# Optimization experiments

Measured on AMD Instinct MI355X. Metric: run time of the kernel, lower is better.

## Reference

```python
import jax, jax.numpy as jnp
import numpy as np

NUM_NODES = 20000
EMB_DIM = 128
HIDDEN = 64
NUM_RELS = 8
NUM_CLASSES = 16
HEADS = 3
NUM_EDGES = 640000
NEG_SLOPE = 0.2


def setup_inputs() -> dict:
    key = jax.random.key(0)
    ks = jax.random.split(key, 12)
    edge_index = jax.random.randint(ks[0], (2, NUM_EDGES), 0, NUM_NODES, dtype=jnp.int32)
    edge_type = jax.random.randint(ks[1], (NUM_EDGES,), 0, NUM_RELS, dtype=jnp.int32)
    s1 = 1.0 / np.sqrt(EMB_DIM)
    s2 = 1.0 / np.sqrt(HIDDEN)
    return {
        "emb": jax.random.normal(ks[2], (NUM_NODES, EMB_DIM), jnp.float32),
        "w1": jax.random.normal(ks[3], (NUM_RELS, EMB_DIM, HEADS * HIDDEN), jnp.float32) * s1,
        "q1": jax.random.normal(ks[4], (HEADS * HIDDEN, HEADS), jnp.float32) * s2,
        "k1": jax.random.normal(ks[5], (HEADS * HIDDEN, HEADS), jnp.float32) * s2,
        "b1": jnp.zeros((HIDDEN,), jnp.float32),
        "w2": jax.random.normal(ks[6], (NUM_RELS, HIDDEN, HEADS * NUM_CLASSES), jnp.float32) * s2,
        "q2": jax.random.normal(ks[7], (HEADS * NUM_CLASSES, HEADS), jnp.float32) * 0.1,
        "k2": jax.random.normal(ks[8], (HEADS * NUM_CLASSES, HEADS), jnp.float32) * 0.1,
        "b2": jnp.zeros((NUM_CLASSES,), jnp.float32),
        "edge_index": edge_index,
        "edge_type": edge_type,
    }


def _rgat_conv(x, w, q, k, b, src, dst, edge_type, heads, out_ch):
    # Per-relation node transform [R, N, heads*out]; equivalent to x_e @ w[edge_type[e]]
    n = x.shape[0]
    xr = jnp.einsum('nd,rdo->rno', x, w)
    out_i = xr[edge_type, dst]  # [E, heads*out] (destination, x_i)
    out_j = xr[edge_type, src]  # [E, heads*out] (source, x_j)
    # additive self-attention with dim=1: alpha [E, heads]
    alpha = jax.nn.leaky_relu(out_i @ q + out_j @ k, negative_slope=NEG_SLOPE)
    # across-relation segment softmax over destination index (PyG utils.softmax)
    amax = jax.ops.segment_max(alpha, dst, num_segments=n)
    amax = jnp.where(jnp.isneginf(amax), 0.0, amax)
    ex = jnp.exp(alpha - amax[dst])
    denom = jax.ops.segment_sum(ex, dst, num_segments=n)
    alpha = ex / (denom[dst] + 1e-16)
    # weighted messages, scatter-add aggregation
    msg = alpha[:, :, None] * out_j.reshape(-1, heads, out_ch)  # [E, heads, out]
    aggr = jax.ops.segment_sum(msg, dst, num_segments=n)  # [N, heads, out]
    # concat=False -> mean over heads, then bias [out]
    return aggr.mean(axis=1) + b


def reference(emb, w1, q1, k1, b1, w2, q2, k2, b2, edge_index, edge_type):
    src, dst = edge_index[0], edge_index[1]
    x1 = _rgat_conv(emb, w1, q1, k1, b1, src, dst, edge_type, HEADS, HIDDEN)
    x2 = jax.nn.relu(x1)
    x3 = _rgat_conv(x2, w2, q2, k2, b2, src, dst, edge_type, HEADS, NUM_CLASSES)
    return jax.nn.sigmoid(x3)
```

## Files before the change

kernel.cpp:

```cpp
#include <hip/hip_runtime.h>
#include <hip/hip_bf16.h>
#include <math.h>

#define N_NODES 20000
#define EMB 128
#define HID 64
#define RELS 8
#define CLS 16
#define N_EDGES 640000
#define NEG 0.2f
#define NKEYS (N_NODES * RELS)
#define SCAN_CHUNK 1024
#define SCAN_NBLK ((NKEYS + SCAN_CHUNK - 1) / SCAN_CHUNK)

typedef unsigned short ushort_t;
typedef __attribute__((ext_vector_type(8))) short bf16x8;
typedef __attribute__((ext_vector_type(8))) unsigned short ushort8_t;
typedef __attribute__((ext_vector_type(4))) unsigned short ushort4_t;
typedef __attribute__((ext_vector_type(4))) float f32x4;

__device__ __forceinline__ float b2f(ushort_t u) {
    return __uint_as_float(((unsigned int)u) << 16);
}
__device__ __forceinline__ ushort_t f2b(float f) {
    __hip_bfloat16 h = __float2bfloat16(f);
    return *reinterpret_cast<ushort_t*>(&h);
}

__device__ __forceinline__ void prep_cvt(int i, const float* __restrict__ in, ushort_t* __restrict__ outp) {
    float4 v = *(const float4*)&in[(size_t)i * 4];
    ushort4 o;
    o.x = f2b(v.x); o.y = f2b(v.y); o.z = f2b(v.z); o.w = f2b(v.w);
    *(ushort4*)&outp[(size_t)i * 4] = o;
}

template <int D, int OUT>
__device__ __forceinline__ void prep_wqk(int tid, const float* __restrict__ w, const float* __restrict__ q,
                                         const float* __restrict__ k, ushort_t* __restrict__ wqkt) {
    int c = tid / D, i = tid % D;
    int r = c / 6, j = c % 6;
    const float* qk = (j < 3) ? q : k;
    int jj = (j < 3) ? j : j - 3;
    const float* wrow = w + ((size_t)r * D + i) * OUT;
    float s = 0.f;
    for (int o = 0; o < OUT; o++) s += wrow[o] * qk[o * 3 + jj];
    wqkt[(size_t)c * D + i] = f2b(s);
}

template <int D, int OC>
__device__ __forceinline__ void prep_wagg(int tid, const float* __restrict__ w, ushort_t* __restrict__ outp) {
    const int KT = RELS * 3 * D;
    int kidx = tid % KT;
    int o = tid / KT;
    int r = kidx / (3 * D), h = (kidx / D) % 3, i = kidx % D;
    outp[tid] = f2b(w[((size_t)r * D + i) * (3 * OC) + h * OC + o]);
}

#define PREP_N0 (N_NODES * EMB / 4)
#define PREP_N1 (48 * 128)
#define PREP_N2 (48 * 64)
#define PREP_N3 (64 * 3072)
#define PREP_N4 (16 * 1536)
#define PREP_TOT (PREP_N0 + PREP_N1 + PREP_N2 + PREP_N3 + PREP_N4)

__global__ __launch_bounds__(256) void k_prep(const float* __restrict__ emb, ushort_t* __restrict__ emb_b,
                                              const float* __restrict__ w1, const float* __restrict__ q1,
                                              const float* __restrict__ k1, ushort_t* __restrict__ wqkt1,
                                              const float* __restrict__ w2, const float* __restrict__ q2,
                                              const float* __restrict__ k2, ushort_t* __restrict__ wqkt2,
                                              ushort_t* __restrict__ wagg1, ushort_t* __restrict__ wagg2) {
    int tid = blockIdx.x * 256 + threadIdx.x;
    if (tid < PREP_N0) { prep_cvt(tid, emb, emb_b); return; }
    tid -= PREP_N0;
    if (tid < PREP_N1) { prep_wqk<128, 192>(tid, w1, q1, k1, wqkt1); return; }
    tid -= PREP_N1;
    if (tid < PREP_N2) { prep_wqk<64, 48>(tid, w2, q2, k2, wqkt2); return; }
    tid -= PREP_N2;
    if (tid < PREP_N3) { prep_wagg<128, 64>(tid, w1, wagg1); return; }
    tid -= PREP_N3;
    if (tid < PREP_N4) { prep_wagg<64, 16>(tid, w2, wagg2); return; }
}

__global__ __launch_bounds__(256) void k_count(const int* __restrict__ dst, const int* __restrict__ et,
                                               int* __restrict__ counts) {
    int e = blockIdx.x * blockDim.x + threadIdx.x;
    if (e < N_EDGES) atomicAdd(&counts[dst[e] * 8 + et[e]], 1);
}

__global__ __launch_bounds__(256) void k_scanA(const int* __restrict__ counts, int* __restrict__ keyoff,
                                               int* __restrict__ blocksum) {
    __shared__ int part[256];
    int b = blockIdx.x, tid = threadIdx.x;
    int base = b * SCAN_CHUNK + tid * 4;
    int4 c = make_int4(0, 0, 0, 0);
    if (base + 3 < NKEYS) c = *(const int4*)&counts[base];
    else {
        if (base + 0 < NKEYS) c.x = counts[base + 0];
        if (base + 1 < NKEYS) c.y = counts[base + 1];
        if (base + 2 < NKEYS) c.z = counts[base + 2];
        if (base + 3 < NKEYS) c.w = counts[base + 3];
    }
    int s = c.x + c.y + c.z + c.w;
    part[tid] = s;
    __syncthreads();
    for (int off = 1; off < 256; off <<= 1) {
        int v = (tid >= off) ? part[tid - off] : 0;
        __syncthreads();
        part[tid] += v;
        __syncthreads();
    }
    int excl = part[tid] - s;
    int4 o;
    o.x = excl;
    o.y = excl + c.x;
    o.z = excl + c.x + c.y;
    o.w = excl + c.x + c.y + c.z;
    if (base + 3 < NKEYS) *(int4*)&keyoff[base] = o;
    else {
        if (base + 0 < NKEYS) keyoff[base + 0] = o.x;
        if (base + 1 < NKEYS) keyoff[base + 1] = o.y;
        if (base + 2 < NKEYS) keyoff[base + 2] = o.z;
        if (base + 3 < NKEYS) keyoff[base + 3] = o.w;
    }
    if (tid == 255) blocksum[b] = part[255];
}

__global__ __launch_bounds__(256) void k_scanB(int* __restrict__ blocksum, int* __restrict__ blockbase,
                                               int* __restrict__ keyoff) {
    __shared__ int part[256];
    int tid = threadIdx.x;
    int v0 = (tid < SCAN_NBLK) ? blocksum[tid] : 0;
    part[tid] = v0;
    __syncthreads();
    for (int off = 1; off < 256; off <<= 1) {
        int v = (tid >= off) ? part[tid - off] : 0;
        __syncthreads();
        part[tid] += v;
        __syncthreads();
    }
    if (tid < SCAN_NBLK) blockbase[tid] = part[tid] - v0;
    if (tid == 255) keyoff[NKEYS] = part[255];
}

__global__ __launch_bounds__(256) void k_scanC(const int* __restrict__ blockbase, int* __restrict__ keyoff,
                                               int* __restrict__ cursor) {
    int b = blockIdx.x, tid = threadIdx.x;
    int base = b * SCAN_CHUNK + tid * 4;
    int add = blockbase[b];
    if (base + 3 < NKEYS) {
        int4 v = *(const int4*)&keyoff[base];
        v.x += add; v.y += add; v.z += add; v.w += add;
        *(int4*)&keyoff[base] = v;
        *(int4*)&cursor[base] = v;
    } else {
        for (int j = 0; j < 4; j++) {
            if (base + j < NKEYS) {
                int v = keyoff[base + j] + add;
                keyoff[base + j] = v;
                cursor[base + j] = v;
            }
        }
    }
}

__global__ __launch_bounds__(256) void k_scatter(const int* __restrict__ src, const int* __restrict__ dst,
                                                 const int* __restrict__ et, int* __restrict__ cursor,
                                                 int* __restrict__ srcs) {
    int e = blockIdx.x * blockDim.x + threadIdx.x;
    if (e < N_EDGES) {
        int p = atomicAdd(&cursor[dst[e] * 8 + et[e]], 1);
        srcs[p] = src[e];
    }
}

template <int K, int KCH, int N, int MREP, int NREP>
__global__ __launch_bounds__(256) void k_mfma_gemm(const ushort_t* __restrict__ A, const ushort_t* __restrict__ Bt,
                                                   float* __restrict__ outp, int M) {
    const int wid = threadIdx.x >> 6;
    const int lane = threadIdx.x & 63;
    const int m0 = blockIdx.x * (4 * MREP * 16) + wid * (MREP * 16);
    const int kbase = blockIdx.y * KCH;
    const int l15 = lane & 15;
    const int kq = (lane >> 4) * 8;

    f32x4 acc[MREP][NREP] = {};
    for (int kk = kbase; kk < kbase + KCH; kk += 32) {
        bf16x8 a[MREP], b[NREP];
#pragma unroll
        for (int i = 0; i < MREP; i++) {
            int row = m0 + i * 16 + l15;
            row = row < M ? row : M - 1;
            a[i] = *(const bf16x8*)&A[(size_t)row * K + kk + kq];
        }
#pragma unroll
        for (int j = 0; j < NREP; j++) b[j] = *(const bf16x8*)&Bt[(size_t)(j * 16 + l15) * K + kk + kq];
#pragma unroll
        for (int i = 0; i < MREP; i++)
#pragma unroll
            for (int j = 0; j < NREP; j++)
                acc[i][j] = __builtin_amdgcn_mfma_f32_16x16x32_bf16(a[i], b[j], acc[i][j], 0, 0, 0);
    }
    float* op = outp + (size_t)blockIdx.y * M * N;
    const int r4 = (lane >> 4) * 4;
#pragma unroll
    for (int i = 0; i < MREP; i++) {
#pragma unroll
        for (int j = 0; j < NREP; j++) {
#pragma unroll
            for (int g = 0; g < 4; g++) {
                int row = m0 + i * 16 + r4 + g;
                if (row < M) op[(size_t)row * N + j * 16 + l15] = acc[i][j][g];
            }
        }
    }
}

__device__ __forceinline__ void edge_alpha(int s_idx, const int (&ko)[9], const int* __restrict__ srcs,
                                           const float* __restrict__ qkd, const float* __restrict__ qbase,
                                           float& a0, float& a1, float& a2, int& sv) {
    int r = 0;
#pragma unroll
    for (int j = 1; j < 8; j++) r += (s_idx >= ko[j]) ? 1 : 0;
    sv = srcs[s_idx];
    const float* kd = qkd + (size_t)sv * 48 + r * 6 + 3;
    const float* qd = qbase + r * 6;
    float t0 = qd[0] + kd[0], t1 = qd[1] + kd[1], t2 = qd[2] + kd[2];
    a0 = t0 > 0.f ? t0 : NEG * t0;
    a1 = t1 > 0.f ? t1 : NEG * t1;
    a2 = t2 > 0.f ? t2 : NEG * t2;
}

__global__ __launch_bounds__(256) void k_stats(const int* __restrict__ keyoff, const int* __restrict__ srcs,
                                               const float* __restrict__ qkd, float4* __restrict__ svw) {
    int node = blockIdx.x * 4 + (threadIdx.x >> 6);
    int lane = threadIdx.x & 63;
    int ko[9];
#pragma unroll
    for (int j = 0; j < 9; j++) ko[j] = keyoff[node * 8 + j];
    int beg = ko[0], end = ko[8], deg = end - beg;
    if (deg == 0) return;
    const float* qbase = qkd + (size_t)node * 48;

    if (deg <= 64) {
        float a0 = -INFINITY, a1 = -INFINITY, a2 = -INFINITY;
        int sv = 0;
        if (lane < deg) edge_alpha(beg + lane, ko, srcs, qkd, qbase, a0, a1, a2, sv);
        float m0 = a0, m1 = a1, m2 = a2;
#pragma unroll
        for (int off = 32; off >= 1; off >>= 1) {
            m0 = fmaxf(m0, __shfl_xor(m0, off));
            m1 = fmaxf(m1, __shfl_xor(m1, off));
            m2 = fmaxf(m2, __shfl_xor(m2, off));
        }
        float e0 = 0.f, e1 = 0.f, e2 = 0.f;
        if (lane < deg) {
            e0 = expf(a0 - m0);
            e1 = expf(a1 - m1);
            e2 = expf(a2 - m2);
        }
        float s0 = e0, s1 = e1, s2 = e2;
#pragma unroll
        for (int off = 32; off >= 1; off >>= 1) {
            s0 += __shfl_xor(s0, off);
            s1 += __shfl_xor(s1, off);
            s2 += __shfl_xor(s2, off);
        }
        float i0 = 1.f / (3.f * (s0 + 1e-16f));
        float i1 = 1.f / (3.f * (s1 + 1e-16f));
        float i2 = 1.f / (3.f * (s2 + 1e-16f));
        if (lane < deg)
            svw[beg + lane] = make_float4(__int_as_float(sv), e0 * i0, e1 * i1, e2 * i2);
    } else {
        float m0 = -INFINITY, m1 = -INFINITY, m2 = -INFINITY;
        for (int i = beg + lane; i < end; i += 64) {
            float a0, a1, a2; int sv;
            edge_alpha(i, ko, srcs, qkd, qbase, a0, a1, a2, sv);
            m0 = fmaxf(m0, a0); m1 = fmaxf(m1, a1); m2 = fmaxf(m2, a2);
        }
#pragma unroll
        for (int off = 32; off >= 1; off >>= 1) {
            m0 = fmaxf(m0, __shfl_xor(m0, off));
            m1 = fmaxf(m1, __shfl_xor(m1, off));
            m2 = fmaxf(m2, __shfl_xor(m2, off));
        }
        float s0 = 0.f, s1 = 0.f, s2 = 0.f;
        for (int i = beg + lane; i < end; i += 64) {
            float a0, a1, a2; int sv;
            edge_alpha(i, ko, srcs, qkd, qbase, a0, a1, a2, sv);
            s0 += expf(a0 - m0); s1 += expf(a1 - m1); s2 += expf(a2 - m2);
        }
#pragma unroll
        for (int off = 32; off >= 1; off >>= 1) {
            s0 += __shfl_xor(s0, off);
            s1 += __shfl_xor(s1, off);
            s2 += __shfl_xor(s2, off);
        }
        float i0 = 1.f / (3.f * (s0 + 1e-16f));
        float i1 = 1.f / (3.f * (s1 + 1e-16f));
        float i2 = 1.f / (3.f * (s2 + 1e-16f));
        for (int i = beg + lane; i < end; i += 64) {
            float a0, a1, a2; int sv;
            edge_alpha(i, ko, srcs, qkd, qbase, a0, a1, a2, sv);
            svw[i] = make_float4(__int_as_float(sv), expf(a0 - m0) * i0, expf(a1 - m1) * i1, expf(a2 - m2) * i2);
        }
    }
}

#define PADK1 408
__global__ __launch_bounds__(256) void k_fused1(const int* __restrict__ keyoff, const float4* __restrict__ svw,
                                                const ushort_t* __restrict__ x, const ushort_t* __restrict__ wagg,
                                                float* __restrict__ part) {
    __shared__ ushort_t lt[16][PADK1];
    const int tid = threadIdx.x;
    const int w = tid >> 6, lane = tid & 63;
    const int q15 = lane & 15, kq = (lane >> 4) * 8;
    const int l15 = lane & 15;
    const int nbase = blockIdx.x * 16;
    const int r = blockIdx.y;
    const int mynode = w * 4 + (lane >> 4);
    const int key = (nbase + mynode) * 8 + r;

    const int beg = keyoff[key], end = keyoff[key + 1];
    const int deg = end - beg;
    float a0[8] = {}, a1[8] = {}, a2[8] = {};
    if (deg > 0) {
        float4 sw0 = svw[beg];
        float4 sw1;
        {
            int s = beg + 1;
            sw1 = svw[s < end ? s : beg];
            if (1 >= deg) { sw1.y = 0.f; sw1.z = 0.f; sw1.w = 0.f; }
        }
        ushort8_t xv0 = *(const ushort8_t*)&x[(size_t)__float_as_int(sw0.x) * 128 + q15 * 8];
        for (int i = 0; i < deg; i++) {
            float4 sw2;
            {
                int s = beg + i + 2;
                sw2 = svw[s < end ? s : beg];
                if (i + 2 >= deg) { sw2.y = 0.f; sw2.z = 0.f; sw2.w = 0.f; }
            }
            ushort8_t xv1 = *(const ushort8_t*)&x[(size_t)__float_as_int(sw1.x) * 128 + q15 * 8];
#pragma unroll
            for (int c = 0; c < 8; c++) {
                float f = b2f(xv0[c]);
                a0[c] += sw0.y * f;
                a1[c] += sw0.z * f;
                a2[c] += sw0.w * f;
            }
            sw0 = sw1;
            sw1 = sw2;
            xv0 = xv1;
        }
    }
    ushort8_t o0, o1, o2;
#pragma unroll
    for (int c = 0; c < 8; c++) {
        o0[c] = f2b(a0[c]);
        o1[c] = f2b(a1[c]);
        o2[c] = f2b(a2[c]);
    }
    *(ushort8_t*)&lt[mynode][0 * 128 + q15 * 8] = o0;
    *(ushort8_t*)&lt[mynode][1 * 128 + q15 * 8] = o1;
    *(ushort8_t*)&lt[mynode][2 * 128 + q15 * 8] = o2;
    __syncthreads();

    f32x4 acc = {};
#pragma unroll
    for (int ks = 0; ks < 12; ks++) {
        bf16x8 av = *(const bf16x8*)&lt[l15][ks * 32 + kq];
        bf16x8 bv = *(const bf16x8*)&wagg[(size_t)(w * 16 + l15) * 3072 + r * 384 + ks * 32 + kq];
        acc = __builtin_amdgcn_mfma_f32_16x16x32_bf16(av, bv, acc, 0, 0, 0);
    }
    float* op = part + (size_t)r * N_NODES * 64;
    const int r4 = (lane >> 4) * 4;
#pragma unroll
    for (int g = 0; g < 4; g++) {
        int row = nbase + r4 + g;
        op[(size_t)row * 64 + w * 16 + l15] = acc[g];
    }
}

#define PADK2 208
__global__ __launch_bounds__(256) void k_fused2(const int* __restrict__ keyoff, const float4* __restrict__ svw,
                                                const ushort_t* __restrict__ x2in, const ushort_t* __restrict__ wagg,
                                                float* __restrict__ part) {
    __shared__ ushort_t lt[16][PADK2];
    const int tid = threadIdx.x;
    const int w = tid >> 6, lane = tid & 63;
    const int q15 = lane & 15, kq = (lane >> 4) * 8;
    const int l15 = lane & 15;
    const int nbase = blockIdx.x * 16;
    const int r = blockIdx.y;
    const int mynode = w * 4 + (lane >> 4);
    const int key = (nbase + mynode) * 8 + r;

    const int beg = keyoff[key], end = keyoff[key + 1];
    const int deg = end - beg;
    float a0[4] = {}, a1[4] = {}, a2[4] = {};
    if (deg > 0) {
        float4 sw0 = svw[beg];
        float4 sw1;
        {
            int s = beg + 1;
            sw1 = svw[s < end ? s : beg];
            if (1 >= deg) { sw1.y = 0.f; sw1.z = 0.f; sw1.w = 0.f; }
        }
        ushort4_t xv0 = *(const ushort4_t*)&x2in[(size_t)__float_as_int(sw0.x) * 64 + q15 * 4];
        for (int i = 0; i < deg; i++) {
            float4 sw2;
            {
                int s = beg + i + 2;
                sw2 = svw[s < end ? s : beg];
                if (i + 2 >= deg) { sw2.y = 0.f; sw2.z = 0.f; sw2.w = 0.f; }
            }
            ushort4_t xv1 = *(const ushort4_t*)&x2in[(size_t)__float_as_int(sw1.x) * 64 + q15 * 4];
#pragma unroll
            for (int c = 0; c < 4; c++) {
                float f = b2f(xv0[c]);
                a0[c] += sw0.y * f;
                a1[c] += sw0.z * f;
                a2[c] += sw0.w * f;
            }
            sw0 = sw1;
            sw1 = sw2;
            xv0 = xv1;
        }
    }
    ushort4_t o0, o1, o2;
#pragma unroll
    for (int c = 0; c < 4; c++) {
        o0[c] = f2b(a0[c]);
        o1[c] = f2b(a1[c]);
        o2[c] = f2b(a2[c]);
    }
    *(ushort4_t*)&lt[mynode][0 * 64 + q15 * 4] = o0;
    *(ushort4_t*)&lt[mynode][1 * 64 + q15 * 4] = o1;
    *(ushort4_t*)&lt[mynode][2 * 64 + q15 * 4] = o2;
    __syncthreads();

    if (w == 0) {
        f32x4 acc = {};
#pragma unroll
        for (int ks = 0; ks < 6; ks++) {
            bf16x8 av = *(const bf16x8*)&lt[l15][ks * 32 + kq];
            bf16x8 bv = *(const bf16x8*)&wagg[(size_t)l15 * 1536 + r * 192 + ks * 32 + kq];
            acc = __builtin_amdgcn_mfma_f32_16x16x32_bf16(av, bv, acc, 0, 0, 0);
        }
        const int r4 = (lane >> 4) * 4;
#pragma unroll
        for (int g = 0; g < 4; g++)
            part[(size_t)r * N_NODES * 16 + (size_t)(nbase + r4 + g) * 16 + l15] = acc[g];
    }
}

__global__ __launch_bounds__(256) void k_reduce1(const float* __restrict__ part, const float* __restrict__ bias,
                                                 ushort_t* __restrict__ x2) {
    int idx = blockIdx.x * blockDim.x + threadIdx.x;
    const int MN = N_NODES * 64;
    if (idx >= MN) return;
    float s = bias[idx & 63];
#pragma unroll
    for (int r = 0; r < 8; r++) s += part[idx + (size_t)r * MN];
    x2[idx] = f2b(s > 0.f ? s : 0.f);
}

__global__ __launch_bounds__(256) void k_reduce2(const float* __restrict__ part, const float* __restrict__ bias,
                                                 float* __restrict__ outp) {
    int idx = blockIdx.x * blockDim.x + threadIdx.x;
    const int MN = N_NODES * 16;
    if (idx >= MN) return;
    float s = bias[idx & 15];
#pragma unroll
    for (int r = 0; r < 8; r++) s += part[idx + (size_t)r * MN];
    outp[idx] = 1.f / (1.f + expf(-s));
}

extern "C" void kernel_launch(void* const* d_in, const int* in_sizes, int n_in, void* d_out, int out_size,
                              void* d_ws, size_t ws_size, hipStream_t stream) {
    const float* emb = (const float*)d_in[0];
    const float* w1 = (const float*)d_in[1];
    const float* q1 = (const float*)d_in[2];
    const float* k1 = (const float*)d_in[3];
    const float* b1 = (const float*)d_in[4];
    const float* w2 = (const float*)d_in[5];
    const float* q2 = (const float*)d_in[6];
    const float* k2 = (const float*)d_in[7];
    const float* b2 = (const float*)d_in[8];
    const int* eidx = (const int*)d_in[9];
    const int* etype = (const int*)d_in[10];
    const int* srcv = eidx;
    const int* dstv = eidx + N_EDGES;
    float* out = (float*)d_out;

    char* p = (char*)d_ws;
    auto alloc = [&](size_t bytes) -> void* {
        void* q = p;
        p += (bytes + 255) & ~(size_t)255;
        return q;
    };
    int* counts = (int*)alloc((size_t)NKEYS * 4);
    int* keyoff = (int*)alloc((size_t)(NKEYS + 1) * 4);
    int* cursor = (int*)alloc((size_t)NKEYS * 4);
    int* blocksum = (int*)alloc((size_t)SCAN_NBLK * 4);
    int* blockbase = (int*)alloc((size_t)SCAN_NBLK * 4);
    int* srcs = (int*)alloc((size_t)N_EDGES * 4);
    float4* svw = (float4*)alloc((size_t)N_EDGES * 16);
    ushort_t* emb_b = (ushort_t*)alloc((size_t)N_NODES * EMB * 2);
    ushort_t* wqkt1 = (ushort_t*)alloc((size_t)48 * 128 * 2);
    ushort_t* wagg1 = (ushort_t*)alloc((size_t)64 * 3072 * 2);
    ushort_t* wqkt2 = (ushort_t*)alloc((size_t)48 * 64 * 2);
    ushort_t* wagg2 = (ushort_t*)alloc((size_t)16 * 1536 * 2);
    float* qkd = (float*)alloc((size_t)N_NODES * 48 * 4);
    ushort_t* x2 = (ushort_t*)alloc((size_t)N_NODES * 64 * 2);
    float* partials = (float*)alloc((size_t)8 * N_NODES * 64 * 4);

    k_prep<<<(PREP_TOT + 255) / 256, 256, 0, stream>>>(emb, emb_b, w1, q1, k1, wqkt1, w2, q2, k2, wqkt2, wagg1,
                                                       wagg2);

    hipMemsetAsync(counts, 0, (size_t)NKEYS * 4, stream);
    k_count<<<(N_EDGES + 255) / 256, 256, 0, stream>>>(dstv, etype, counts);
    k_scanA<<<SCAN_NBLK, 256, 0, stream>>>(counts, keyoff, blocksum);
    k_scanB<<<1, 256, 0, stream>>>(blocksum, blockbase, keyoff);
    k_scanC<<<SCAN_NBLK, 256, 0, stream>>>(blockbase, keyoff, cursor);
    k_scatter<<<(N_EDGES + 255) / 256, 256, 0, stream>>>(srcv, dstv, etype, cursor, srcs);

    k_mfma_gemm<128, 128, 48, 1, 3><<<dim3(313, 1), 256, 0, stream>>>(emb_b, wqkt1, qkd, N_NODES);
    k_stats<<<N_NODES / 4, 256, 0, stream>>>(keyoff, srcs, qkd, svw);
    k_fused1<<<dim3(N_NODES / 16, 8), 256, 0, stream>>>(keyoff, svw, emb_b, wagg1, partials);
    k_reduce1<<<(N_NODES * 64 + 255) / 256, 256, 0, stream>>>(partials, b1, x2);

    k_mfma_gemm<64, 64, 48, 1, 3><<<dim3(313, 1), 256, 0, stream>>>(x2, wqkt2, qkd, N_NODES);
    k_stats<<<N_NODES / 4, 256, 0, stream>>>(keyoff, srcs, qkd, svw);
    k_fused2<<<dim3(N_NODES / 16, 8), 256, 0, stream>>>(keyoff, svw, x2, wagg2, partials);
    k_reduce2<<<(N_NODES * 16 + 255) / 256, 256, 0, stream>>>(partials, b2, out);
}
```

Before: 243.8 us.

## Stage first gathered neighbor rows into LDS via global_load_lds before aggregation

In both fused aggregation kernels, each wave issues asynchronous global-to-LDS loads for up to 8 source rows per (node, relation) key up front, then waits once and accumulates from LDS. Edges beyond 8 fall back to direct global loads without the previous software prefetch pipeline. This aims to expose more memory-level parallelism for the irregular gather instead of a serial dependent-load chain. It adds LDS usage (which may lower occupancy) and a full vmcnt wait before any compute.

```diff
diff --git a/kernel.cpp b/kernel.cpp
--- a/kernel.cpp
+++ b/kernel.cpp
@@ -12,6 +12,7 @@
 #define NKEYS (N_NODES * RELS)
 #define SCAN_CHUNK 1024
 #define SCAN_NBLK ((NKEYS + SCAN_CHUNK - 1) / SCAN_CHUNK)
+#define S1ROWS 8
 
 typedef unsigned short ushort_t;
 typedef __attribute__((ext_vector_type(8))) short bf16x8;
@@ -25,6 +26,11 @@
 __device__ __forceinline__ ushort_t f2b(float f) {
     __hip_bfloat16 h = __float2bfloat16(f);
     return *reinterpret_cast<ushort_t*>(&h);
+}
+
+__device__ __forceinline__ void gload_lds16(const ushort_t* g, ushort_t* l) {
+    __builtin_amdgcn_global_load_lds((const __attribute__((address_space(1))) void*)g,
+                                     (__attribute__((address_space(3))) void*)l, 16, 0, 0);
 }
 
 __device__ __forceinline__ void prep_cvt(int i, const float* __restrict__ in, ushort_t* __restrict__ outp) {
@@ -307,9 +313,10 @@
 }
 
 #define PADK1 408
-__global__ __launch_bounds__(256) void k_fused1(const int* __restrict__ keyoff, const float4* __restrict__ svw,
-                                                const ushort_t* __restrict__ x, const ushort_t* __restrict__ wagg,
-                                                float* __restrict__ part) {
+__global__ __launch_bounds__(256) void k_fused1(const int* __restrict__ keyoff, const int* __restrict__ srcs,
+                                                const float4* __restrict__ svw, const ushort_t* __restrict__ x,
+                                                const ushort_t* __restrict__ wagg, float* __restrict__ part) {
+    __shared__ ushort_t stage[4][32][128];
     __shared__ ushort_t lt[16][PADK1];
     const int tid = threadIdx.x;
     const int w = tid >> 6, lane = tid & 63;
@@ -317,39 +324,54 @@
     const int l15 = lane & 15;
     const int nbase = blockIdx.x * 16;
     const int r = blockIdx.y;
-    const int mynode = w * 4 + (lane >> 4);
+    const int ln16 = lane >> 4;
+    const int mynode = w * 4 + ln16;
     const int key = (nbase + mynode) * 8 + r;
-
     const int beg = keyoff[key], end = keyoff[key + 1];
     const int deg = end - beg;
+
+#pragma unroll
+    for (int qq = 0; qq < 4; qq++) {
+        int kqk = (nbase + w * 4 + qq) * 8 + r;
+        int b = keyoff[kqk];
+        int en = keyoff[kqk + 1];
+        int nst = en - b;
+        nst = nst < S1ROWS ? nst : S1ROWS;
+#pragma unroll
+        for (int ii = 0; ii < 2; ii++) {
+            if (ii * 4 < nst) {
+                int jloc = ii * 4 + ln16;
+                int j = b + (jloc < nst ? jloc : 0);
+                int sj = srcs[j];
+                gload_lds16(&x[(size_t)sj * 128 + q15 * 8], &stage[w][qq * 8 + ii * 4][0]);
+            }
+        }
+    }
+    asm volatile("s_waitcnt vmcnt(0)" ::: "memory");
+    __builtin_amdgcn_sched_barrier(0);
+
     float a0[8] = {}, a1[8] = {}, a2[8] = {};
-    if (deg > 0) {
-        float4 sw0 = svw[beg];
-        float4 sw1;
-        {
-            int s = beg + 1;
-            sw1 = svw[s < end ? s : beg];
-            if (1 >= deg) { sw1.y = 0.f; sw1.z = 0.f; sw1.w = 0.f; }
-        }
-        ushort8_t xv0 = *(const ushort8_t*)&x[(size_t)__float_as_int(sw0.x) * 128 + q15 * 8];
-        for (int i = 0; i < deg; i++) {
-            float4 sw2;
-            {
-                int s = beg + i + 2;
-                sw2 = svw[s < end ? s : beg];
-                if (i + 2 >= deg) { sw2.y = 0.f; sw2.z = 0.f; sw2.w = 0.f; }
-            }
-            ushort8_t xv1 = *(const ushort8_t*)&x[(size_t)__float_as_int(sw1.x) * 128 + q15 * 8];
-#pragma unroll
-            for (int c = 0; c < 8; c++) {
-                float f = b2f(xv0[c]);
-                a0[c] += sw0.y * f;
-                a1[c] += sw0.z * f;
-                a2[c] += sw0.w * f;
-            }
-            sw0 = sw1;
-            sw1 = sw2;
-            xv0 = xv1;
+    const int nst = deg < S1ROWS ? deg : S1ROWS;
+    for (int j = 0; j < nst; j++) {
+        float4 sw = svw[beg + j];
+        ushort8_t xv = *(const ushort8_t*)&stage[w][ln16 * 8 + j][q15 * 8];
+#pragma unroll
+        for (int c = 0; c < 8; c++) {
+            float f = b2f(xv[c]);
+            a0[c] += sw.y * f;
+            a1[c] += sw.z * f;
+            a2[c] += sw.w * f;
+        }
+    }
+    for (int s = beg + S1ROWS; s < end; s++) {
+        float4 sw = svw[s];
+        ushort8_t xv = *(const ushort8_t*)&x[(size_t)__float_as_int(sw.x) * 128 + q15 * 8];
+#pragma unroll
+        for (int c = 0; c < 8; c++) {
+            float f = b2f(xv[c]);
+            a0[c] += sw.y * f;
+            a1[c] += sw.z * f;
+            a2[c] += sw.w * f;
         }
     }
     ushort8_t o0, o1, o2;
@@ -381,9 +403,10 @@
 }
 
 #define PADK2 208
-__global__ __launch_bounds__(256) void k_fused2(const int* __restrict__ keyoff, const float4* __restrict__ svw,
-                                                const ushort_t* __restrict__ x2in, const ushort_t* __restrict__ wagg,
-                                                float* __restrict__ part) {
+__global__ __launch_bounds__(256) void k_fused2(const int* __restrict__ keyoff, const int* __restrict__ srcs,
+                                                const float4* __restrict__ svw, const ushort_t* __restrict__ x2in,
+                                                const ushort_t* __restrict__ wagg, float* __restrict__ part) {
+    __shared__ ushort_t stage[4][32][64];
     __shared__ ushort_t lt[16][PADK2];
     const int tid = threadIdx.x;
     const int w = tid >> 6, lane = tid & 63;
@@ -391,39 +414,52 @@
     const int l15 = lane & 15;
     const int nbase = blockIdx.x * 16;
     const int r = blockIdx.y;
-    const int mynode = w * 4 + (lane >> 4);
+    const int ln16 = lane >> 4;
+    const int mynode = w * 4 + ln16;
     const int key = (nbase + mynode) * 8 + r;
-
     const int beg = keyoff[key], end = keyoff[key + 1];
     const int deg = end - beg;
+
+    const int e8 = lane >> 3;
+    const int c8 = lane & 7;
+#pragma unroll
+    for (int qq = 0; qq < 4; qq++) {
+        int kqk = (nbase + w * 4 + qq) * 8 + r;
+        int b = keyoff[kqk];
+        int en = keyoff[kqk + 1];
+        int nst = en - b;
+        nst = nst < S1ROWS ? nst : S1ROWS;
+        if (nst > 0) {
+            int j = b + (e8 < nst ? e8 : 0);
+            int sj = srcs[j];
+            gload_lds16(&x2in[(size_t)sj * 64 + c8 * 8], &stage[w][qq * 8][0]);
+        }
+    }
+    asm volatile("s_waitcnt vmcnt(0)" ::: "memory");
+    __builtin_amdgcn_sched_barrier(0);
+
     float a0[4] = {}, a1[4] = {}, a2[4] = {};
-    if (deg > 0) {
-        float4 sw0 = svw[beg];
-        float4 sw1;
-        {
-            int s = beg + 1;
-            sw1 = svw[s < end ? s : beg];
-            if (1 >= deg) { sw1.y = 0.f; sw1.z = 0.f; sw1.w = 0.f; }
-        }
-        ushort4_t xv0 = *(const ushort4_t*)&x2in[(size_t)__float_as_int(sw0.x) * 64 + q15 * 4];
-        for (int i = 0; i < deg; i++) {
-            float4 sw2;
-            {
-                int s = beg + i + 2;
-                sw2 = svw[s < end ? s : beg];
-                if (i + 2 >= deg) { sw2.y = 0.f; sw2.z = 0.f; sw2.w = 0.f; }
-            }
-            ushort4_t xv1 = *(const ushort4_t*)&x2in[(size_t)__float_as_int(sw1.x) * 64 + q15 * 4];
-#pragma unroll
-            for (int c = 0; c < 4; c++) {
-                float f = b2f(xv0[c]);
-                a0[c] += sw0.y * f;
-                a1[c] += sw0.z * f;
-                a2[c] += sw0.w * f;
-            }
-            sw0 = sw1;
-            sw1 = sw2;
-            xv0 = xv1;
+    const int nst = deg < S1ROWS ? deg : S1ROWS;
+    for (int j = 0; j < nst; j++) {
+        float4 sw = svw[beg + j];
+        ushort4_t xv = *(const ushort4_t*)&stage[w][ln16 * 8 + j][q15 * 4];
+#pragma unroll
+        for (int c = 0; c < 4; c++) {
+            float f = b2f(xv[c]);
+            a0[c] += sw.y * f;
+            a1[c] += sw.z * f;
+            a2[c] += sw.w * f;
+        }
+    }
+    for (int s = beg + S1ROWS; s < end; s++) {
+        float4 sw = svw[s];
+        ushort4_t xv = *(const ushort4_t*)&x2in[(size_t)__float_as_int(sw.x) * 64 + q15 * 4];
+#pragma unroll
+        for (int c = 0; c < 4; c++) {
+            float f = b2f(xv[c]);
+            a0[c] += sw.y * f;
+            a1[c] += sw.z * f;
+            a2[c] += sw.w * f;
         }
     }
     ushort4_t o0, o1, o2;
@@ -526,11 +562,11 @@
 
     k_mfma_gemm<128, 128, 48, 1, 3><<<dim3(313, 1), 256, 0, stream>>>(emb_b, wqkt1, qkd, N_NODES);
     k_stats<<<N_NODES / 4, 256, 0, stream>>>(keyoff, srcs, qkd, svw);
-    k_fused1<<<dim3(N_NODES / 16, 8), 256, 0, stream>>>(keyoff, svw, emb_b, wagg1, partials);
+    k_fused1<<<dim3(N_NODES / 16, 8), 256, 0, stream>>>(keyoff, srcs, svw, emb_b, wagg1, partials);
     k_reduce1<<<(N_NODES * 64 + 255) / 256, 256, 0, stream>>>(partials, b1, x2);
 
     k_mfma_gemm<64, 64, 48, 1, 3><<<dim3(313, 1), 256, 0, stream>>>(x2, wqkt2, qkd, N_NODES);
     k_stats<<<N_NODES / 4, 256, 0, stream>>>(keyoff, srcs, qkd, svw);
-    k_fused2<<<dim3(N_NODES / 16, 8), 256, 0, stream>>>(keyoff, svw, x2, wagg2, partials);
+    k_fused2<<<dim3(N_NODES / 16, 8), 256, 0, stream>>>(keyoff, srcs, svw, x2, wagg2, partials);
     k_reduce2<<<(N_NODES * 16 + 255) / 256, 256, 0, stream>>>(partials, b2, out);
 }
```

Result: slower. 299.7 us (+22.9%).

## Split layer-1 edge gather across two wave groups per node-relation key

Applied to the files above, without the earlier changes.

k_fused1 now launches 512 threads, and two groups of four waves each process alternate edges (even/odd) of every (node, relation) segment into separate LDS tiles. The MFMA stage then sums both partial tiles by issuing two MFMAs per k-step in the first four waves. The goal is to halve the serial gather chain per thread and expose more memory-level parallelism on the long dependent load loop. In exchange, half the waves sit idle during the MFMA phase, LDS use doubles, and the two partial sums are each rounded to bf16 before the GEMM.

```diff
diff --git a/kernel.cpp b/kernel.cpp
--- a/kernel.cpp
+++ b/kernel.cpp
@@ -307,49 +307,46 @@
 }
 
 #define PADK1 408
-__global__ __launch_bounds__(256) void k_fused1(const int* __restrict__ keyoff, const float4* __restrict__ svw,
+__global__ __launch_bounds__(512) void k_fused1(const int* __restrict__ keyoff, const float4* __restrict__ svw,
                                                 const ushort_t* __restrict__ x, const ushort_t* __restrict__ wagg,
                                                 float* __restrict__ part) {
-    __shared__ ushort_t lt[16][PADK1];
+    __shared__ ushort_t lt[2][16][PADK1];
     const int tid = threadIdx.x;
     const int w = tid >> 6, lane = tid & 63;
     const int q15 = lane & 15, kq = (lane >> 4) * 8;
     const int l15 = lane & 15;
     const int nbase = blockIdx.x * 16;
     const int r = blockIdx.y;
-    const int mynode = w * 4 + (lane >> 4);
+    const int mynode = (w & 3) * 4 + (lane >> 4);
+    const int p = w >> 2;
     const int key = (nbase + mynode) * 8 + r;
 
     const int beg = keyoff[key], end = keyoff[key + 1];
-    const int deg = end - beg;
     float a0[8] = {}, a1[8] = {}, a2[8] = {};
-    if (deg > 0) {
-        float4 sw0 = svw[beg];
-        float4 sw1;
-        {
-            int s = beg + 1;
-            sw1 = svw[s < end ? s : beg];
-            if (1 >= deg) { sw1.y = 0.f; sw1.z = 0.f; sw1.w = 0.f; }
-        }
-        ushort8_t xv0 = *(const ushort8_t*)&x[(size_t)__float_as_int(sw0.x) * 128 + q15 * 8];
-        for (int i = 0; i < deg; i++) {
-            float4 sw2;
-            {
-                int s = beg + i + 2;
-                sw2 = svw[s < end ? s : beg];
-                if (i + 2 >= deg) { sw2.y = 0.f; sw2.z = 0.f; sw2.w = 0.f; }
+    {
+        int sA = beg + p;
+        if (sA < end) {
+            float4 sw0 = svw[sA];
+            int sB = sA + 2;
+            float4 sw1 = svw[sB < end ? sB : beg];
+            if (sB >= end) { sw1.y = 0.f; sw1.z = 0.f; sw1.w = 0.f; }
+            ushort8_t xv0 = *(const ushort8_t*)&x[(size_t)__float_as_int(sw0.x) * 128 + q15 * 8];
+            for (int s = sA; s < end; s += 2) {
+                int sC = s + 4;
+                float4 sw2 = svw[sC < end ? sC : beg];
+                if (sC >= end) { sw2.y = 0.f; sw2.z = 0.f; sw2.w = 0.f; }
+                ushort8_t xv1 = *(const ushort8_t*)&x[(size_t)__float_as_int(sw1.x) * 128 + q15 * 8];
+#pragma unroll
+                for (int c = 0; c < 8; c++) {
+                    float f = b2f(xv0[c]);
+                    a0[c] += sw0.y * f;
+                    a1[c] += sw0.z * f;
+                    a2[c] += sw0.w * f;
+                }
+                sw0 = sw1;
+                sw1 = sw2;
+                xv0 = xv1;
             }
-            ushort8_t xv1 = *(const ushort8_t*)&x[(size_t)__float_as_int(sw1.x) * 128 + q15 * 8];
-#pragma unroll
-            for (int c = 0; c < 8; c++) {
-                float f = b2f(xv0[c]);
-                a0[c] += sw0.y * f;
-                a1[c] += sw0.z * f;
-                a2[c] += sw0.w * f;
-            }
-            sw0 = sw1;
-            sw1 = sw2;
-            xv0 = xv1;
         }
     }
     ushort8_t o0, o1, o2;
@@ -359,24 +356,28 @@
         o1[c] = f2b(a1[c]);
         o2[c] = f2b(a2[c]);
     }
-    *(ushort8_t*)&lt[mynode][0 * 128 + q15 * 8] = o0;
-    *(ushort8_t*)&lt[mynode][1 * 128 + q15 * 8] = o1;
-    *(ushort8_t*)&lt[mynode][2 * 128 + q15 * 8] = o2;
+    *(ushort8_t*)&lt[p][mynode][0 * 128 + q15 * 8] = o0;
+    *(ushort8_t*)&lt[p][mynode][1 * 128 + q15 * 8] = o1;
+    *(ushort8_t*)&lt[p][mynode][2 * 128 + q15 * 8] = o2;
     __syncthreads();
 
-    f32x4 acc = {};
-#pragma unroll
-    for (int ks = 0; ks < 12; ks++) {
-        bf16x8 av = *(const bf16x8*)&lt[l15][ks * 32 + kq];
-        bf16x8 bv = *(const bf16x8*)&wagg[(size_t)(w * 16 + l15) * 3072 + r * 384 + ks * 32 + kq];
-        acc = __builtin_amdgcn_mfma_f32_16x16x32_bf16(av, bv, acc, 0, 0, 0);
-    }
-    float* op = part + (size_t)r * N_NODES * 64;
-    const int r4 = (lane >> 4) * 4;
-#pragma unroll
-    for (int g = 0; g < 4; g++) {
-        int row = nbase + r4 + g;
-        op[(size_t)row * 64 + w * 16 + l15] = acc[g];
+    if (w < 4) {
+        f32x4 acc = {};
+#pragma unroll
+        for (int ks = 0; ks < 12; ks++) {
+            bf16x8 bv = *(const bf16x8*)&wagg[(size_t)(w * 16 + l15) * 3072 + r * 384 + ks * 32 + kq];
+            bf16x8 av0 = *(const bf16x8*)&lt[0][l15][ks * 32 + kq];
+            bf16x8 av1 = *(const bf16x8*)&lt[1][l15][ks * 32 + kq];
+            acc = __builtin_amdgcn_mfma_f32_16x16x32_bf16(av0, bv, acc, 0, 0, 0);
+            acc = __builtin_amdgcn_mfma_f32_16x16x32_bf16(av1, bv, acc, 0, 0, 0);
+        }
+        float* op = part + (size_t)r * N_NODES * 64;
+        const int r4 = (lane >> 4) * 4;
+#pragma unroll
+        for (int g = 0; g < 4; g++) {
+            int row = nbase + r4 + g;
+            op[(size_t)row * 64 + w * 16 + l15] = acc[g];
+        }
     }
 }
 
@@ -526,7 +527,7 @@
 
     k_mfma_gemm<128, 128, 48, 1, 3><<<dim3(313, 1), 256, 0, stream>>>(emb_b, wqkt1, qkd, N_NODES);
     k_stats<<<N_NODES / 4, 256, 0, stream>>>(keyoff, srcs, qkd, svw);
-    k_fused1<<<dim3(N_NODES / 16, 8), 256, 0, stream>>>(keyoff, svw, emb_b, wagg1, partials);
+    k_fused1<<<dim3(N_NODES / 16, 8), 512, 0, stream>>>(keyoff, svw, emb_b, wagg1, partials);
     k_reduce1<<<(N_NODES * 64 + 255) / 256, 256, 0, stream>>>(partials, b1, x2);
 
     k_mfma_gemm<64, 64, 48, 1, 3><<<dim3(313, 1), 256, 0, stream>>>(x2, wqkt2, qkd, N_NODES);
```

Measured after the change: 247.2 us. About the same (+1.4%).
